# Kernel optimization log

Measured on AMD Instinct MI355X. Metric: run time of the kernel, lower is better.

Reference implementation:

```python
import jax, jax.numpy as jnp
import numpy as np


def setup_inputs() -> dict:
    key = jax.random.key(0)
    k1, k2 = jax.random.split(key)
    B, T, D, K = 16, 4096, 1024, 512
    h = jax.random.normal(k1, (B, T, D), dtype=jnp.float32)
    codebook = jax.random.normal(k2, (K, D), dtype=jnp.float32)
    return {"h": h, "codebook": codebook}


def reference(h, codebook):
    """SAMMCodebook.encode: nearest-codeword indices via squared L2 distance.

    h: [B, T, D]; codebook: [K, D] -> z: [B, T] int32
    """
    B, T, D = h.shape
    h_flat = h.reshape(-1, D)                                  # [N, D]
    h_sq = jnp.sum(h_flat * h_flat, axis=-1, keepdims=True)    # [N, 1]
    c_sq = jnp.sum(codebook * codebook, axis=-1)[None, :]      # [1, K]
    # dist[n,k] = ||h_n||^2 + ||c_k||^2 - 2 <h_n, c_k>
    dist = h_sq + c_sq - 2.0 * (h_flat @ codebook.T)           # [N, K]
    z = jnp.argmin(dist, axis=-1).reshape(B, T)
    return z.astype(jnp.int32)
```

## Files before the change

kernel.cpp:

```cpp
#include <hip/hip_runtime.h>


#define D_DIM 1024
#define K_CB  512
#define DELTA 4.0f
#define MAXC  8
#define SENT  0xFFFFu

typedef __attribute__((ext_vector_type(8))) short short8;
typedef __attribute__((ext_vector_type(4))) float floatx4;

#define WS_CBB  0ull
#define WS_CSQ  1048576ull
#define WS_SLOT 1050624ull
#define WS_WL   3147776ull
#define WS_CNT  3409920ull

typedef const unsigned int __attribute__((address_space(1)))* gaddr_t;
typedef unsigned int __attribute__((address_space(3)))* laddr_t;
static __device__ __forceinline__ void async_copy16(const void* g, void* l) {
    __builtin_amdgcn_global_load_lds((gaddr_t)g, (laddr_t)l, 16, 0, 0);
}

static __device__ __forceinline__ unsigned f2bf(float f) {
    unsigned u = __builtin_bit_cast(unsigned, f);
    return (u + 0x7FFFu + ((u >> 16) & 1u)) >> 16;
}

__global__ __launch_bounds__(256)
void prep_kernel(const float* __restrict__ cb, unsigned short* __restrict__ cbb,
                 float* __restrict__ csq) {
    __shared__ float red[4];
    const int k = blockIdx.x, t = threadIdx.x;
    const float4 v = *(const float4*)(cb + (size_t)k * D_DIM + t * 4);
    uint2 u;
    u.x = f2bf(v.x) | (f2bf(v.y) << 16);
    u.y = f2bf(v.z) | (f2bf(v.w) << 16);
    *(uint2*)(cbb + (size_t)k * D_DIM + t * 4) = u;
    float s = v.x * v.x + v.y * v.y + v.z * v.z + v.w * v.w;
    #pragma unroll
    for (int off = 32; off > 0; off >>= 1) s += __shfl_down(s, off, 64);
    if ((t & 63) == 0) red[t >> 6] = s;
    __syncthreads();
    if (t == 0) csq[k] = red[0] + red[1] + red[2] + red[3];
}

__global__ __launch_bounds__(256, 2)
void coarse_kernel(const float* __restrict__ h,
                   const unsigned short* __restrict__ cbb,
                   const float* __restrict__ csq,
                   uint4* __restrict__ slots,
                   int* __restrict__ wl,
                   unsigned* __restrict__ wcount,
                   int* __restrict__ out) {
    __shared__ unsigned char smem[66560] __attribute__((aligned(16)));
    unsigned short* As = (unsigned short*)smem;
    unsigned short* Bs = (unsigned short*)(smem + 4096);

    const int tid = threadIdx.x;
    const int w = tid >> 6, lane = tid & 63;
    const int l15 = lane & 15, kq = lane >> 4;
    const size_t row0 = (size_t)blockIdx.x * 64;
    const int wc_ = w * 128;

    const int ar = tid >> 2, adq = (tid & 3) * 8;
    const float* gA = h + (row0 + ar) * D_DIM + adq;
    const unsigned short* gB0 = cbb + (size_t)(tid >> 2) * D_DIM + (tid & 3) * 8;
    unsigned short* ldsB0 = Bs + (size_t)(w * 64 + (lane)) * 0;

    floatx4 acc[4][8];
    #pragma unroll
    for (int i = 0; i < 4; ++i)
        #pragma unroll
        for (int j = 0; j < 8; ++j) acc[i][j] = (floatx4){0.f, 0.f, 0.f, 0.f};

    for (int dk = 0; dk < D_DIM; dk += 32) {
        #pragma unroll
        for (int j = 0; j < 8; ++j)
            async_copy16(gB0 + (size_t)j * 64 * D_DIM + dk,
                         Bs + (size_t)(j * 256 + w * 64) * 8);
        const float4 v0 = *(const float4*)(gA + dk);
        const float4 v1 = *(const float4*)(gA + dk + 4);
        uint4 u;
        u.x = f2bf(v0.x) | (f2bf(v0.y) << 16);
        u.y = f2bf(v0.z) | (f2bf(v0.w) << 16);
        u.z = f2bf(v1.x) | (f2bf(v1.y) << 16);
        u.w = f2bf(v1.z) | (f2bf(v1.w) << 16);
        *(uint4*)(As + ar * 32 + adq) = u;
        __syncthreads();

        short8 a[4], b[8];
        #pragma unroll
        for (int rt = 0; rt < 4; ++rt)
            a[rt] = *(const short8*)(As + (rt * 16 + l15) * 32 + kq * 8);
        #pragma unroll
        for (int ct = 0; ct < 8; ++ct)
            b[ct] = *(const short8*)(Bs + (wc_ + ct * 16 + l15) * 32 + kq * 8);
        #pragma unroll
        for (int rt = 0; rt < 4; ++rt)
            #pragma unroll
            for (int ct = 0; ct < 8; ++ct)
                acc[rt][ct] = __builtin_amdgcn_mfma_f32_16x16x32_bf16(
                    a[rt], b[ct], acc[rt][ct], 0, 0, 0);
        __syncthreads();
    }

    float k1[16], k2[16];
    unsigned cpk[16];
    #pragma unroll
    for (int i = 0; i < 16; ++i) { k1[i] = 3.4e38f; k2[i] = 3.4e38f; cpk[i] = 0; }
    #pragma unroll
    for (int ct = 0; ct < 8; ++ct) {
        const int col = wc_ + ct * 16 + l15;
        const float cq = csq[col];
        #pragma unroll
        for (int rt = 0; rt < 4; ++rt)
            #pragma unroll
            for (int reg = 0; reg < 4; ++reg) {
                const float s = fmaf(-2.0f, acc[rt][ct][reg], cq);
                const int ri = rt * 4 + reg;
                if (s < k1[ri]) {
                    k2[ri] = k1[ri]; k1[ri] = s;
                    cpk[ri] = (cpk[ri] << 16) | (unsigned)col;
                } else if (s < k2[ri]) {
                    k2[ri] = s;
                    cpk[ri] = (cpk[ri] & 0xFFFFu) | ((unsigned)col << 16);
                }
            }
    }

    float* mval = (float*)smem;
    int*   mcol = (int*)(smem + 33280);
    __syncthreads();
    #pragma unroll
    for (int rt = 0; rt < 4; ++rt)
        #pragma unroll
        for (int reg = 0; reg < 4; ++reg) {
            const int ri = rt * 4 + reg;
            const int r = rt * 16 + kq * 4 + reg;
            const int e = (w * 16 + l15) * 2;
            mval[r * 130 + e] = k1[ri];
            mcol[r * 130 + e] = (int)(cpk[ri] & 0xFFFFu);
            mval[r * 130 + e + 1] = k2[ri];
            mcol[r * 130 + e + 1] = (int)(cpk[ri] >> 16);
        }
    __syncthreads();

    if (tid < 64) {
        const int r = tid;
        float bv = mval[r * 130]; int bc = mcol[r * 130];
        for (int e = 1; e < 128; ++e) {
            const float v = mval[r * 130 + e];
            const int   c = mcol[r * 130 + e];
            if (v < bv || (v == bv && c < bc)) { bv = v; bc = c; }
        }
        const float thr = bv + DELTA;
        unsigned cd[MAXC] = {0, 0, 0, 0, 0, 0, 0, 0};
        int others = 0;
        for (int e = 0; e < 128; ++e) {
            const float v = mval[r * 130 + e];
            const int   c = mcol[r * 130 + e];
            if (v < thr && c != bc) {
                if (others < MAXC) cd[others] = (unsigned)c;
                ++others;
            }
        }
        const size_t grow = row0 + r;
        if (others == 0) {
            out[grow] = bc;
        } else {
            const unsigned cnt = (others > MAXC) ? SENT : (unsigned)others;
            uint4 s0, s1;
            s0.x = __builtin_bit_cast(unsigned, bv);
            s0.y = (unsigned)bc | (cnt << 16);
            s0.z = cd[0] | (cd[1] << 16);
            s0.w = cd[2] | (cd[3] << 16);
            s1.x = cd[4] | (cd[5] << 16);
            s1.y = cd[6] | (cd[7] << 16);
            s1.z = 0; s1.w = 0;
            slots[grow * 2] = s0;
            slots[grow * 2 + 1] = s1;
            wl[atomicAdd(wcount, 1u)] = (int)grow;
        }
    }
}

__global__ __launch_bounds__(256)
void fixup_kernel(const float* __restrict__ h, const float* __restrict__ cb,
                  const float* __restrict__ csq, const uint4* __restrict__ slots,
                  const int* __restrict__ wl, const unsigned* __restrict__ wcount,
                  int* __restrict__ out) {
    const int w = threadIdx.x >> 6, lane = threadIdx.x & 63;
    const unsigned idx = blockIdx.x * 4 + w;
    if (idx >= *wcount) return;
    const size_t row = (size_t)wl[idx];
    const uint4 s0 = slots[row * 2];
    const uint4 s1 = slots[row * 2 + 1];
    const unsigned cnt = s0.y >> 16;
    const bool full = (cnt == SENT);
    int cl[1 + MAXC]; int nc = 0;
    if (!full) {
        cl[0] = (int)(s0.y & 0xFFFFu);
        const unsigned cds[MAXC] = {s0.z & 0xFFFFu, s0.z >> 16, s0.w & 0xFFFFu, s0.w >> 16,
                                    s1.x & 0xFFFFu, s1.x >> 16, s1.y & 0xFFFFu, s1.y >> 16};
        nc = 1 + (int)cnt;
        #pragma unroll
        for (int i = 0; i < MAXC; ++i)
            if (i < (int)cnt) cl[1 + i] = (int)cds[i];
    }

    const float* hrow = h + row * D_DIM;
    float4 hv[4];
    #pragma unroll
    for (int j = 0; j < 4; ++j)
        hv[j] = *(const float4*)(hrow + j * 256 + lane * 4);

    float bs = 3.4e38f; int bc = 0x7fffffff;
    const int total = full ? K_CB : nc;
    for (int i = 0; i < total; ++i) {
        const int c = full ? i : cl[i];
        const float* crow = cb + (size_t)c * D_DIM;
        float d = 0.0f;
        #pragma unroll
        for (int j = 0; j < 4; ++j) {
            const float4 cv = *(const float4*)(crow + j * 256 + lane * 4);
            d = fmaf(hv[j].x, cv.x, d);
            d = fmaf(hv[j].y, cv.y, d);
            d = fmaf(hv[j].z, cv.z, d);
            d = fmaf(hv[j].w, cv.w, d);
        }
        #pragma unroll
        for (int off = 32; off > 0; off >>= 1) d += __shfl_down(d, off, 64);
        d = __shfl(d, 0, 64);
        const float sc = fmaf(-2.0f, d, csq[c]);
        if (sc < bs || (sc == bs && c < bc)) { bs = sc; bc = c; }
    }
    if (lane == 0) out[row] = bc;
}

extern "C" void kernel_launch(void* const* d_in, const int* in_sizes, int n_in,
                              void* d_out, int out_size, void* d_ws, size_t ws_size,
                              hipStream_t stream) {
    const float* h  = (const float*)d_in[0];
    const float* cb = (const float*)d_in[1];
    int* out = (int*)d_out;
    unsigned char* ws = (unsigned char*)d_ws;
    const int nrows = in_sizes[0] / D_DIM;

    unsigned short* cbb = (unsigned short*)(ws + WS_CBB);
    float* csq   = (float*)(ws + WS_CSQ);
    uint4* slots = (uint4*)(ws + WS_SLOT);
    int*   wl    = (int*)(ws + WS_WL);
    unsigned* wc = (unsigned*)(ws + WS_CNT);

    hipMemsetAsync(wc, 0, 4, stream);
    prep_kernel<<<dim3(K_CB), dim3(256), 0, stream>>>(cb, cbb, csq);
    coarse_kernel<<<dim3(nrows / 64), dim3(256), 0, stream>>>(
        h, cbb, csq, slots, wl, wc, out);
    fixup_kernel<<<dim3(nrows / 4), dim3(256), 0, stream>>>(
        h, cb, csq, slots, wl, wc, out);
}
```

Measured before the change: 483.0 us.

## Double-buffer coarse GEMM with swizzled LDS and fuse fp32 fixup into coarse kernel

The coarse bf16 MFMA loop now double-buffers A and B tiles in LDS. The next tile's global and async loads are issued before the current tile's MFMAs, which leaves one barrier per step, and LDS addresses are XOR-swizzled to cut bank conflicts. The separate fixup kernel, the memset and the global worklist with its atomics are removed. Ambiguous rows are now rescored exactly in fp32 inside the coarse kernel using an LDS candidate list that holds up to 15 candidates. This costs more LDS per block, which may lower occupancy, and leaves the fused rescoring tail imbalanced across blocks.

```diff
diff --git a/kernel.cpp b/kernel.cpp
--- a/kernel.cpp
+++ b/kernel.cpp
@@ -4,17 +4,14 @@
 #define D_DIM 1024
 #define K_CB  512
 #define DELTA 4.0f
-#define MAXC  8
-#define SENT  0xFFFFu
+#define MAXC_IN 15
+#define FULLSCAN 0xFFFFu
 
 typedef __attribute__((ext_vector_type(8))) short short8;
 typedef __attribute__((ext_vector_type(4))) float floatx4;
 
 #define WS_CBB  0ull
 #define WS_CSQ  1048576ull
-#define WS_SLOT 1050624ull
-#define WS_WL   3147776ull
-#define WS_CNT  3409920ull
 
 typedef const unsigned int __attribute__((address_space(1)))* gaddr_t;
 typedef unsigned int __attribute__((address_space(3)))* laddr_t;
@@ -49,13 +46,11 @@
 void coarse_kernel(const float* __restrict__ h,
                    const unsigned short* __restrict__ cbb,
                    const float* __restrict__ csq,
-                   uint4* __restrict__ slots,
-                   int* __restrict__ wl,
-                   unsigned* __restrict__ wcount,
+                   const float* __restrict__ cb,
                    int* __restrict__ out) {
-    __shared__ unsigned char smem[66560] __attribute__((aligned(16)));
+    __shared__ unsigned char smem[73728] __attribute__((aligned(16)));
     unsigned short* As = (unsigned short*)smem;
-    unsigned short* Bs = (unsigned short*)(smem + 4096);
+    unsigned short* Bs = (unsigned short*)(smem + 8192);
 
     const int tid = threadIdx.x;
     const int w = tid >> 6, lane = tid & 63;
@@ -63,10 +58,15 @@
     const size_t row0 = (size_t)blockIdx.x * 64;
     const int wc_ = w * 128;
 
-    const int ar = tid >> 2, adq = (tid & 3) * 8;
-    const float* gA = h + (row0 + ar) * D_DIM + adq;
-    const unsigned short* gB0 = cbb + (size_t)(tid >> 2) * D_DIM + (tid & 3) * 8;
-    unsigned short* ldsB0 = Bs + (size_t)(w * 64 + (lane)) * 0;
+    const int qp8 = (kq ^ ((l15 >> 1) & 3)) * 8;
+
+    const int ar = tid >> 2, aql = tid & 3;
+    const float* gA = h + (row0 + ar) * D_DIM + aql * 8;
+    const int awoff = ar * 32 + (aql ^ ((ar >> 1) & 3)) * 8;
+
+    const int qsrc = (tid & 3) ^ ((tid >> 3) & 3);
+    const unsigned char* cbb_b = (const unsigned char*)cbb;
+    const size_t bsrc0 = ((size_t)(tid >> 2) * D_DIM + qsrc * 8) * 2;
 
     floatx4 acc[4][8];
     #pragma unroll
@@ -74,35 +74,61 @@
         #pragma unroll
         for (int j = 0; j < 8; ++j) acc[i][j] = (floatx4){0.f, 0.f, 0.f, 0.f};
 
-    for (int dk = 0; dk < D_DIM; dk += 32) {
+    {
+        const floatx4 va0 = __builtin_nontemporal_load((const floatx4*)gA);
+        const floatx4 va1 = __builtin_nontemporal_load((const floatx4*)(gA + 4));
         #pragma unroll
         for (int j = 0; j < 8; ++j)
-            async_copy16(gB0 + (size_t)j * 64 * D_DIM + dk,
-                         Bs + (size_t)(j * 256 + w * 64) * 8);
-        const float4 v0 = *(const float4*)(gA + dk);
-        const float4 v1 = *(const float4*)(gA + dk + 4);
+            async_copy16(cbb_b + bsrc0 + (size_t)j * 64 * D_DIM * 2,
+                         Bs + (size_t)j * 2048 + w * 512);
         uint4 u;
-        u.x = f2bf(v0.x) | (f2bf(v0.y) << 16);
-        u.y = f2bf(v0.z) | (f2bf(v0.w) << 16);
-        u.z = f2bf(v1.x) | (f2bf(v1.y) << 16);
-        u.w = f2bf(v1.z) | (f2bf(v1.w) << 16);
-        *(uint4*)(As + ar * 32 + adq) = u;
+        u.x = f2bf(va0.x) | (f2bf(va0.y) << 16);
+        u.y = f2bf(va0.z) | (f2bf(va0.w) << 16);
+        u.z = f2bf(va1.x) | (f2bf(va1.y) << 16);
+        u.w = f2bf(va1.z) | (f2bf(va1.w) << 16);
+        *(uint4*)(As + awoff) = u;
         __syncthreads();
-
+    }
+
+    int cur = 0;
+    for (int s = 0; s < 32; ++s) {
+        floatx4 vb0, vb1;
+        const int dn = (s + 1) * 32;
+        if (s < 31) {
+            vb0 = __builtin_nontemporal_load((const floatx4*)(gA + dn));
+            vb1 = __builtin_nontemporal_load((const floatx4*)(gA + dn + 4));
+            #pragma unroll
+            for (int j = 0; j < 8; ++j)
+                async_copy16(cbb_b + bsrc0 + (size_t)j * 64 * D_DIM * 2 + (size_t)dn * 2,
+                             Bs + (cur ^ 1) * 16384 + (size_t)j * 2048 + w * 512);
+        }
+
+        const unsigned short* Asc = As + cur * 2048;
+        const unsigned short* Bsc = Bs + cur * 16384;
         short8 a[4], b[8];
         #pragma unroll
         for (int rt = 0; rt < 4; ++rt)
-            a[rt] = *(const short8*)(As + (rt * 16 + l15) * 32 + kq * 8);
+            a[rt] = *(const short8*)(Asc + (rt * 16 + l15) * 32 + qp8);
         #pragma unroll
         for (int ct = 0; ct < 8; ++ct)
-            b[ct] = *(const short8*)(Bs + (wc_ + ct * 16 + l15) * 32 + kq * 8);
+            b[ct] = *(const short8*)(Bsc + (wc_ + ct * 16 + l15) * 32 + qp8);
         #pragma unroll
         for (int rt = 0; rt < 4; ++rt)
             #pragma unroll
             for (int ct = 0; ct < 8; ++ct)
                 acc[rt][ct] = __builtin_amdgcn_mfma_f32_16x16x32_bf16(
                     a[rt], b[ct], acc[rt][ct], 0, 0, 0);
+
+        if (s < 31) {
+            uint4 u;
+            u.x = f2bf(vb0.x) | (f2bf(vb0.y) << 16);
+            u.y = f2bf(vb0.z) | (f2bf(vb0.w) << 16);
+            u.z = f2bf(vb1.x) | (f2bf(vb1.y) << 16);
+            u.w = f2bf(vb1.z) | (f2bf(vb1.w) << 16);
+            *(uint4*)(As + (cur ^ 1) * 2048 + awoff) = u;
+        }
         __syncthreads();
+        cur ^= 1;
     }
 
     float k1[16], k2[16];
@@ -130,7 +156,9 @@
     }
 
     float* mval = (float*)smem;
-    int*   mcol = (int*)(smem + 33280);
+    int*   mcol = (int*)(smem + 33024);
+    unsigned short* ccnt  = (unsigned short*)(smem + 66048);
+    unsigned short* clist = (unsigned short*)(smem + 66176);
     __syncthreads();
     #pragma unroll
     for (int rt = 0; rt < 4; ++rt)
@@ -139,103 +167,75 @@
             const int ri = rt * 4 + reg;
             const int r = rt * 16 + kq * 4 + reg;
             const int e = (w * 16 + l15) * 2;
-            mval[r * 130 + e] = k1[ri];
-            mcol[r * 130 + e] = (int)(cpk[ri] & 0xFFFFu);
-            mval[r * 130 + e + 1] = k2[ri];
-            mcol[r * 130 + e + 1] = (int)(cpk[ri] >> 16);
+            mval[r * 129 + e] = k1[ri];
+            mcol[r * 129 + e] = (int)(cpk[ri] & 0xFFFFu);
+            mval[r * 129 + e + 1] = k2[ri];
+            mcol[r * 129 + e + 1] = (int)(cpk[ri] >> 16);
         }
     __syncthreads();
 
     if (tid < 64) {
         const int r = tid;
-        float bv = mval[r * 130]; int bc = mcol[r * 130];
+        float bv = mval[r * 129]; int bc = mcol[r * 129];
         for (int e = 1; e < 128; ++e) {
-            const float v = mval[r * 130 + e];
-            const int   c = mcol[r * 130 + e];
+            const float v = mval[r * 129 + e];
+            const int   c = mcol[r * 129 + e];
             if (v < bv || (v == bv && c < bc)) { bv = v; bc = c; }
         }
         const float thr = bv + DELTA;
-        unsigned cd[MAXC] = {0, 0, 0, 0, 0, 0, 0, 0};
         int others = 0;
         for (int e = 0; e < 128; ++e) {
-            const float v = mval[r * 130 + e];
-            const int   c = mcol[r * 130 + e];
+            const float v = mval[r * 129 + e];
+            const int   c = mcol[r * 129 + e];
             if (v < thr && c != bc) {
-                if (others < MAXC) cd[others] = (unsigned)c;
+                if (others < MAXC_IN) clist[r * 16 + 1 + others] = (unsigned short)c;
                 ++others;
             }
         }
+        if (others == 0) {
+            out[row0 + r] = bc;
+            ccnt[r] = 0;
+        } else if (others <= MAXC_IN) {
+            clist[r * 16] = (unsigned short)bc;
+            ccnt[r] = (unsigned short)(others + 1);
+        } else {
+            ccnt[r] = (unsigned short)FULLSCAN;
+        }
+    }
+    __syncthreads();
+
+    for (int r = w; r < 64; r += 4) {
+        const unsigned cnt = ccnt[r];
+        if (cnt == 0) continue;
         const size_t grow = row0 + r;
-        if (others == 0) {
-            out[grow] = bc;
-        } else {
-            const unsigned cnt = (others > MAXC) ? SENT : (unsigned)others;
-            uint4 s0, s1;
-            s0.x = __builtin_bit_cast(unsigned, bv);
-            s0.y = (unsigned)bc | (cnt << 16);
-            s0.z = cd[0] | (cd[1] << 16);
-            s0.w = cd[2] | (cd[3] << 16);
-            s1.x = cd[4] | (cd[5] << 16);
-            s1.y = cd[6] | (cd[7] << 16);
-            s1.z = 0; s1.w = 0;
-            slots[grow * 2] = s0;
-            slots[grow * 2 + 1] = s1;
-            wl[atomicAdd(wcount, 1u)] = (int)grow;
-        }
-    }
-}
-
-__global__ __launch_bounds__(256)
-void fixup_kernel(const float* __restrict__ h, const float* __restrict__ cb,
-                  const float* __restrict__ csq, const uint4* __restrict__ slots,
-                  const int* __restrict__ wl, const unsigned* __restrict__ wcount,
-                  int* __restrict__ out) {
-    const int w = threadIdx.x >> 6, lane = threadIdx.x & 63;
-    const unsigned idx = blockIdx.x * 4 + w;
-    if (idx >= *wcount) return;
-    const size_t row = (size_t)wl[idx];
-    const uint4 s0 = slots[row * 2];
-    const uint4 s1 = slots[row * 2 + 1];
-    const unsigned cnt = s0.y >> 16;
-    const bool full = (cnt == SENT);
-    int cl[1 + MAXC]; int nc = 0;
-    if (!full) {
-        cl[0] = (int)(s0.y & 0xFFFFu);
-        const unsigned cds[MAXC] = {s0.z & 0xFFFFu, s0.z >> 16, s0.w & 0xFFFFu, s0.w >> 16,
-                                    s1.x & 0xFFFFu, s1.x >> 16, s1.y & 0xFFFFu, s1.y >> 16};
-        nc = 1 + (int)cnt;
-        #pragma unroll
-        for (int i = 0; i < MAXC; ++i)
-            if (i < (int)cnt) cl[1 + i] = (int)cds[i];
-    }
-
-    const float* hrow = h + row * D_DIM;
-    float4 hv[4];
-    #pragma unroll
-    for (int j = 0; j < 4; ++j)
-        hv[j] = *(const float4*)(hrow + j * 256 + lane * 4);
-
-    float bs = 3.4e38f; int bc = 0x7fffffff;
-    const int total = full ? K_CB : nc;
-    for (int i = 0; i < total; ++i) {
-        const int c = full ? i : cl[i];
-        const float* crow = cb + (size_t)c * D_DIM;
-        float d = 0.0f;
-        #pragma unroll
-        for (int j = 0; j < 4; ++j) {
-            const float4 cv = *(const float4*)(crow + j * 256 + lane * 4);
-            d = fmaf(hv[j].x, cv.x, d);
-            d = fmaf(hv[j].y, cv.y, d);
-            d = fmaf(hv[j].z, cv.z, d);
-            d = fmaf(hv[j].w, cv.w, d);
-        }
-        #pragma unroll
-        for (int off = 32; off > 0; off >>= 1) d += __shfl_down(d, off, 64);
-        d = __shfl(d, 0, 64);
-        const float sc = fmaf(-2.0f, d, csq[c]);
-        if (sc < bs || (sc == bs && c < bc)) { bs = sc; bc = c; }
-    }
-    if (lane == 0) out[row] = bc;
+        const float* hrow = h + grow * D_DIM;
+        float4 hv[4];
+        #pragma unroll
+        for (int j = 0; j < 4; ++j)
+            hv[j] = *(const float4*)(hrow + j * 256 + lane * 4);
+        float bs = 3.4e38f; int bc = 0x7fffffff;
+        const bool full = (cnt == FULLSCAN);
+        const int total = full ? K_CB : (int)cnt;
+        for (int i = 0; i < total; ++i) {
+            const int c = full ? i : (int)clist[r * 16 + i];
+            const float* crow = cb + (size_t)c * D_DIM;
+            float d = 0.0f;
+            #pragma unroll
+            for (int j = 0; j < 4; ++j) {
+                const float4 cv = *(const float4*)(crow + j * 256 + lane * 4);
+                d = fmaf(hv[j].x, cv.x, d);
+                d = fmaf(hv[j].y, cv.y, d);
+                d = fmaf(hv[j].z, cv.z, d);
+                d = fmaf(hv[j].w, cv.w, d);
+            }
+            #pragma unroll
+            for (int off = 32; off > 0; off >>= 1) d += __shfl_down(d, off, 64);
+            d = __shfl(d, 0, 64);
+            const float sc = fmaf(-2.0f, d, csq[c]);
+            if (sc < bs || (sc == bs && c < bc)) { bs = sc; bc = c; }
+        }
+        if (lane == 0) out[grow] = bc;
+    }
 }
 
 extern "C" void kernel_launch(void* const* d_in, const int* in_sizes, int n_in,
@@ -248,15 +248,9 @@
     const int nrows = in_sizes[0] / D_DIM;
 
     unsigned short* cbb = (unsigned short*)(ws + WS_CBB);
-    float* csq   = (float*)(ws + WS_CSQ);
-    uint4* slots = (uint4*)(ws + WS_SLOT);
-    int*   wl    = (int*)(ws + WS_WL);
-    unsigned* wc = (unsigned*)(ws + WS_CNT);
-
-    hipMemsetAsync(wc, 0, 4, stream);
+    float* csq = (float*)(ws + WS_CSQ);
+
     prep_kernel<<<dim3(K_CB), dim3(256), 0, stream>>>(cb, cbb, csq);
     coarse_kernel<<<dim3(nrows / 64), dim3(256), 0, stream>>>(
-        h, cbb, csq, slots, wl, wc, out);
-    fixup_kernel<<<dim3(nrows / 4), dim3(256), 0, stream>>>(
-        h, cb, csq, slots, wl, wc, out);
-}
+        h, cbb, csq, cb, out);
+}
```

Result: no change. 482.6 us (-0.1%).
